# Kernel optimization log

Hardware: AMD Instinct MI355X
Metric: run time of the kernel (lower is better)

## Reference

```python
import jax, jax.numpy as jnp
import numpy as np

B, S, H, NH, HD, L, I, M = 2, 2048, 768, 12, 64, 6, 3072, 256
VOCAB, TYPES = 30522, 2
EPS = 1e-6  # layernorm epsilon and FAVOR+ numerical stabilizer


def layer_norm(x, g, b):
    mu = jnp.mean(x, axis=-1, keepdims=True)
    var = jnp.mean(jax.lax.square(x), axis=-1, keepdims=True) - jax.lax.square(mu)
    return (x - mu) * jax.lax.rsqrt(var + EPS) * g + b


def favor_attention(q, k, v, mask, proj):
    # q,k,v: [B,S,NH,HD]; proj: [M,HD] random features; mask: [B,S] float
    dn = 1.0 / np.sqrt(np.sqrt(HD))      # data normalizer for softmax kernel
    ratio = 1.0 / np.sqrt(M)
    qn, kn = q * dn, k * dn
    qp = jnp.einsum('bsnd,md->bsnm', qn, proj)
    kp = jnp.einsum('bsnd,md->bsnm', kn, proj)
    qd = 0.5 * jnp.sum(qn * qn, axis=-1, keepdims=True)
    kd = 0.5 * jnp.sum(kn * kn, axis=-1, keepdims=True)
    # stabilizers: per-position max for queries, global (seq+feature) max for keys
    q_prime = ratio * (jnp.exp(qp - qd - jnp.max(qp, axis=-1, keepdims=True)) + EPS)
    k_prime = ratio * (jnp.exp(kp - kd - jnp.max(kp, axis=(1, 3), keepdims=True)) + EPS)
    k_prime = k_prime * mask[:, :, None, None]
    kv = jnp.einsum('bsnm,bsnd->bnmd', k_prime, v)          # [B,NH,M,HD]
    num = jnp.einsum('bsnm,bnmd->bsnd', q_prime, kv)        # [B,S,NH,HD]
    den = jnp.einsum('bsnm,bnm->bsn', q_prime, jnp.sum(k_prime, axis=1))
    return num / den[..., None]


def setup_inputs() -> dict:
    key = jax.random.key(0)
    ks = jax.random.split(key, 32)
    f = lambda i, shape, s=0.02: (jax.random.normal(ks[i], shape, jnp.float32) * s)
    inp = {
        'input_ids': jax.random.randint(ks[0], (B, S), 0, VOCAB, jnp.int32),
        'token_type_ids': jax.random.randint(ks[1], (B, S), 0, TYPES, jnp.int32),
        'position_ids': jnp.tile(jnp.arange(S, dtype=jnp.int32)[None, :], (B, 1)),
        'attention_mask': jnp.ones((B, S), jnp.int32),
        'word_emb': f(2, (VOCAB, H), 0.1),
        'pos_emb': f(3, (S, H), 0.1),
        'type_emb': f(4, (TYPES, H), 0.1),
        'emb_ln_g': jnp.ones((H,), jnp.float32),
        'emb_ln_b': jnp.zeros((H,), jnp.float32),
        'wq': f(5, (L, H, NH, HD)), 'bq': jnp.zeros((L, NH, HD), jnp.float32),
        'wk': f(6, (L, H, NH, HD)), 'bk': jnp.zeros((L, NH, HD), jnp.float32),
        'wv': f(7, (L, H, NH, HD)), 'bv': jnp.zeros((L, NH, HD), jnp.float32),
        'wo': f(8, (L, NH, HD, H)), 'bo': jnp.zeros((L, H), jnp.float32),
        'ln1_g': jnp.ones((L, H), jnp.float32), 'ln1_b': jnp.zeros((L, H), jnp.float32),
        'wi': f(9, (L, H, I)), 'bi': jnp.zeros((L, I), jnp.float32),
        'wo2': f(10, (L, I, H)), 'bo2': jnp.zeros((L, H), jnp.float32),
        'ln2_g': jnp.ones((L, H), jnp.float32), 'ln2_b': jnp.zeros((L, H), jnp.float32),
        'proj': jax.random.normal(ks[11], (L, M, HD), jnp.float32),
    }
    return inp


def reference(input_ids, token_type_ids, position_ids, attention_mask,
              word_emb, pos_emb, type_emb, emb_ln_g, emb_ln_b,
              wq, bq, wk, bk, wv, bv, wo, bo, ln1_g, ln1_b,
              wi, bi, wo2, bo2, ln2_g, ln2_b, proj):
    mask = attention_mask.astype(jnp.float32)
    x = word_emb[input_ids] + pos_emb[position_ids] + type_emb[token_type_ids]
    x = layer_norm(x, emb_ln_g, emb_ln_b)
    for l in range(L):
        q = jnp.einsum('bsh,hnd->bsnd', x, wq[l]) + bq[l]
        k = jnp.einsum('bsh,hnd->bsnd', x, wk[l]) + bk[l]
        v = jnp.einsum('bsh,hnd->bsnd', x, wv[l]) + bv[l]
        att = favor_attention(q, k, v, mask, proj[l])
        att = jnp.einsum('bsnd,ndh->bsh', att, wo[l]) + bo[l]
        a = layer_norm(att + x, ln1_g[l], ln1_b[l])
        inter = jax.nn.gelu(jnp.einsum('bsh,hi->bsi', a, wi[l]) + bi[l])
        out = jnp.einsum('bsi,ih->bsh', inter, wo2[l]) + bo2[l]
        x = layer_norm(out + a, ln2_g[l], ln2_b[l])
    return x
```

## Files before the change

### kernel.cpp

```cpp
#include <hip/hip_runtime.h>
#include <hip/hip_bf16.h>

#define B_ 2
#define S_ 2048
#define H_ 768
#define NH_ 12
#define HD_ 64
#define L_ 6
#define I_ 3072
#define M_ 256
#define BS_ 4096
#define R_ 49152
#define NXH_ 3145728
#define EPS_ 1e-6f
#define DN_ 0.35355339059327373f
#define RATIO_ 0.0625f

typedef __attribute__((ext_vector_type(8))) short bf16x8;
typedef __attribute__((ext_vector_type(4))) float f32x4;

__device__ __forceinline__ void gload16(const void* g, void* l) {
    __builtin_amdgcn_global_load_lds(
        (const __attribute__((address_space(1))) void*)g,
        (__attribute__((address_space(3))) void*)l, 16, 0, 0);
}

__device__ __forceinline__ float gelu_f(float x) {
    const float c = 0.7978845608028654f;
    float x3 = x * x * x;
    return 0.5f * x * (1.0f + tanhf(c * (x + 0.044715f * x3)));
}

__device__ __forceinline__ void blockReduceSum2(float& a, float& b) {
    __shared__ float sa[4], sb[4];
    int lane = threadIdx.x & 63, wid = threadIdx.x >> 6;
    #pragma unroll
    for (int off = 32; off; off >>= 1) {
        a += __shfl_down(a, off, 64);
        b += __shfl_down(b, off, 64);
    }
    __syncthreads();
    if (lane == 0) { sa[wid] = a; sb[wid] = b; }
    __syncthreads();
    a = sa[0] + sa[1] + sa[2] + sa[3];
    b = sb[0] + sb[1] + sb[2] + sb[3];
    __syncthreads();
}

__device__ __forceinline__ float blockReduceMax(float v) {
    __shared__ float sm[4];
    int lane = threadIdx.x & 63, wid = threadIdx.x >> 6;
    #pragma unroll
    for (int off = 32; off; off >>= 1) v = fmaxf(v, __shfl_down(v, off, 64));
    __syncthreads();
    if (lane == 0) sm[wid] = v;
    __syncthreads();
    float r = fmaxf(fmaxf(sm[0], sm[1]), fmaxf(sm[2], sm[3]));
    __syncthreads();
    return r;
}

template<int ACT, int OUTMODE>
__global__ __launch_bounds__(256) void gemm_pipe3_kernel(
    const __hip_bfloat16* __restrict__ A, const __hip_bfloat16* __restrict__ BT,
    const float* __restrict__ bias, void* __restrict__ Cv,
    int K, int lda, int ldb, int ldc, float* __restrict__ aux)
{
    __shared__ __align__(16) unsigned short As[3][128][32];
    __shared__ __align__(16) unsigned short Bs[3][128][32];
    const int tid = threadIdx.x, lane = tid & 63, wid = tid >> 6;
    const int wr = wid >> 1, wc = wid & 1;
    const size_t r0 = (size_t)blockIdx.y * 128;
    const int n0 = blockIdx.x * 128;
    const size_t kbase = (size_t)blockIdx.z * (size_t)K;

    const int srow = lane >> 2;
    const int selem = ((lane & 3) ^ ((srow >> 1) & 3)) * 8;
    const unsigned short* ga0 = (const unsigned short*)A + (r0 + wid * 32 + srow) * (size_t)lda + kbase + selem;
    const unsigned short* gb0 = (const unsigned short*)BT + ((size_t)n0 + wid * 32 + srow) * (size_t)ldb + kbase + selem;

    f32x4 acc[4][4];
    #pragma unroll
    for (int i = 0; i < 4; i++)
        #pragma unroll
        for (int j = 0; j < 4; j++)
            acc[i][j] = (f32x4){0.f, 0.f, 0.f, 0.f};

    const int lr = lane & 15;
    const int rc8 = (((lane >> 4) ^ ((lr >> 1) & 3))) * 8;

#define STAGE_(t) { const int bb_ = (t) % 3; const int kk_ = (t) * 32;            \
    gload16(ga0 + kk_, &As[bb_][wid * 32][0]);                                    \
    gload16(ga0 + kk_ + 16 * (size_t)lda, &As[bb_][wid * 32 + 16][0]);            \
    gload16(gb0 + kk_, &Bs[bb_][wid * 32][0]);                                    \
    gload16(gb0 + kk_ + 16 * (size_t)ldb, &Bs[bb_][wid * 32 + 16][0]); }

#define ITER_(t, VMSTR, DOSTAGE) {                                                \
    if (DOSTAGE) STAGE_((t) + 2);                                                 \
    asm volatile("s_waitcnt vmcnt(" VMSTR ")" ::: "memory");                      \
    __builtin_amdgcn_sched_barrier(0);                                            \
    __builtin_amdgcn_s_barrier();                                                 \
    __builtin_amdgcn_sched_barrier(0);                                            \
    const int bb_ = (t) % 3;                                                      \
    bf16x8 af[4], bfv[4];                                                         \
    _Pragma("unroll") for (int i = 0; i < 4; i++)                                 \
        af[i] = *(const bf16x8*)&As[bb_][wr * 64 + i * 16 + lr][rc8];             \
    _Pragma("unroll") for (int j = 0; j < 4; j++)                                 \
        bfv[j] = *(const bf16x8*)&Bs[bb_][wc * 64 + j * 16 + lr][rc8];            \
    __builtin_amdgcn_s_setprio(1);                                                \
    _Pragma("unroll") for (int i = 0; i < 4; i++)                                 \
        _Pragma("unroll") for (int j = 0; j < 4; j++)                             \
            acc[i][j] = __builtin_amdgcn_mfma_f32_16x16x32_bf16(af[i], bfv[j], acc[i][j], 0, 0, 0); \
    __builtin_amdgcn_s_setprio(0);                                                \
    __builtin_amdgcn_s_barrier();                                                 \
    __builtin_amdgcn_sched_barrier(0); }

    const int nT = K >> 5;
    STAGE_(0); STAGE_(1);
    for (int t = 0; t < nT - 2; ++t) ITER_(t, "8", true);
    ITER_(nT - 2, "4", false);
    ITER_(nT - 1, "0", false);
#undef ITER_
#undef STAGE_

    const int rr = (lane >> 4) * 4;
    const int cc = lane & 15;
    if (OUTMODE == 3) {
        float* fpl = aux + (size_t)blockIdx.z * NXH_;
        #pragma unroll
        for (int i = 0; i < 4; i++) {
            #pragma unroll
            for (int j = 0; j < 4; j++) {
                size_t col = (size_t)n0 + wc * 64 + j * 16 + cc;
                #pragma unroll
                for (int rg = 0; rg < 4; rg++) {
                    size_t row = r0 + wr * 64 + i * 16 + rr + rg;
                    fpl[row * (size_t)ldc + col] = acc[i][j][rg];
                }
            }
        }
    } else if (OUTMODE == 1) {
        #pragma unroll
        for (int i = 0; i < 4; i++) {
            #pragma unroll
            for (int j = 0; j < 4; j++) {
                size_t col = (size_t)n0 + wc * 64 + j * 16 + cc;
                float bv_ = bias ? bias[col] : 0.f;
                #pragma unroll
                for (int rg = 0; rg < 4; rg++) {
                    size_t row = r0 + wr * 64 + i * 16 + rr + rg;
                    float v = acc[i][j][rg] + bv_;
                    if (ACT == 1) v = gelu_f(v);
                    ((__hip_bfloat16*)Cv)[row * (size_t)ldc + col] = __float2bfloat16(v);
                }
            }
        }
    } else {
        const size_t seg = (size_t)n0 / 768;
        const int colbase = n0 - (int)seg * 768;
        #pragma unroll
        for (int i = 0; i < 4; i++) {
            #pragma unroll
            for (int rg = 0; rg < 4; rg++) {
                size_t row = r0 + wr * 64 + i * 16 + rr + rg;
                float ss = 0.f;
                #pragma unroll
                for (int j = 0; j < 4; j++) {
                    int colw = wc * 64 + j * 16 + cc;
                    size_t col = (size_t)n0 + colw;
                    float bv_ = bias ? bias[col] : 0.f;
                    float v = acc[i][j][rg] + bv_;
                    __hip_bfloat16 hb = __float2bfloat16(v);
                    ((__hip_bfloat16*)Cv)[seg * (size_t)NXH_ + row * 768 + colbase + colw] = hb;
                    float vr = __bfloat162float(hb);
                    ss += vr * vr;
                }
                #pragma unroll
                for (int off = 1; off <= 8; off <<= 1)
                    ss += __shfl_xor(ss, off, 64);
                if (seg < 2 && (lane & 15) == 0) {
                    int nh = colbase / 64 + wc;
                    aux[seg * (size_t)R_ + row * 12 + nh] = 0.5f * DN_ * DN_ * ss;
                }
            }
        }
    }
}

__global__ __launch_bounds__(256) void gemm_pipe3_n64_kernel(
    const __hip_bfloat16* __restrict__ A, const __hip_bfloat16* __restrict__ BT,
    const float* __restrict__ bias, float* __restrict__ C,
    int K, int lda, int ldb, int ldc)
{
    __shared__ __align__(16) unsigned short As[3][128][32];
    __shared__ __align__(16) unsigned short Bs[3][64][32];
    const int tid = threadIdx.x, lane = tid & 63, wid = tid >> 6;
    const size_t r0 = (size_t)blockIdx.y * 128;
    const int n0 = blockIdx.x * 64;

    const int srow = lane >> 2;
    const int selem = ((lane & 3) ^ ((srow >> 1) & 3)) * 8;
    const unsigned short* ga0 = (const unsigned short*)A + (r0 + wid * 32 + srow) * (size_t)lda + selem;
    const unsigned short* gb0 = (const unsigned short*)BT + ((size_t)n0 + wid * 16 + srow) * (size_t)ldb + selem;

    f32x4 acc[2][4];
    #pragma unroll
    for (int i = 0; i < 2; i++)
        #pragma unroll
        for (int j = 0; j < 4; j++)
            acc[i][j] = (f32x4){0.f, 0.f, 0.f, 0.f};

    const int lr = lane & 15;
    const int rc8 = (((lane >> 4) ^ ((lr >> 1) & 3))) * 8;

#define STAGE_(t) { const int bb_ = (t) % 3; const int kk_ = (t) * 32;            \
    gload16(ga0 + kk_, &As[bb_][wid * 32][0]);                                    \
    gload16(ga0 + kk_ + 16 * (size_t)lda, &As[bb_][wid * 32 + 16][0]);            \
    gload16(gb0 + kk_, &Bs[bb_][wid * 16][0]); }

#define ITER_(t, VMSTR, DOSTAGE) {                                                \
    if (DOSTAGE) STAGE_((t) + 2);                                                 \
    asm volatile("s_waitcnt vmcnt(" VMSTR ")" ::: "memory");                      \
    __builtin_amdgcn_sched_barrier(0);                                            \
    __builtin_amdgcn_s_barrier();                                                 \
    __builtin_amdgcn_sched_barrier(0);                                            \
    const int bb_ = (t) % 3;                                                      \
    bf16x8 af[2], bfv[4];                                                         \
    _Pragma("unroll") for (int i = 0; i < 2; i++)                                 \
        af[i] = *(const bf16x8*)&As[bb_][wid * 32 + i * 16 + lr][rc8];            \
    _Pragma("unroll") for (int j = 0; j < 4; j++)                                 \
        bfv[j] = *(const bf16x8*)&Bs[bb_][j * 16 + lr][rc8];                      \
    __builtin_amdgcn_s_setprio(1);                                                \
    _Pragma("unroll") for (int i = 0; i < 2; i++)                                 \
        _Pragma("unroll") for (int j = 0; j < 4; j++)                             \
            acc[i][j] = __builtin_amdgcn_mfma_f32_16x16x32_bf16(af[i], bfv[j], acc[i][j], 0, 0, 0); \
    __builtin_amdgcn_s_setprio(0);                                                \
    __builtin_amdgcn_s_barrier();                                                 \
    __builtin_amdgcn_sched_barrier(0); }

    const int nT = K >> 5;
    STAGE_(0); STAGE_(1);
    for (int t = 0; t < nT - 2; ++t) ITER_(t, "6", true);
    ITER_(nT - 2, "3", false);
    ITER_(nT - 1, "0", false);
#undef ITER_
#undef STAGE_

    const int rr = (lane >> 4) * 4, cc = lane & 15;
    #pragma unroll
    for (int i = 0; i < 2; i++) {
        #pragma unroll
        for (int j = 0; j < 4; j++) {
            int col = n0 + j * 16 + cc;
            float bv_ = bias ? bias[col] : 0.f;
            #pragma unroll
            for (int rg = 0; rg < 4; rg++) {
                size_t row = r0 + wid * 32 + i * 16 + rr + rg;
                C[row * (size_t)ldc + col] = acc[i][j][rg] + bv_;
            }
        }
    }
}

__global__ __launch_bounds__(256) void gemm_projk_kernel(
    const __hip_bfloat16* __restrict__ A, const __hip_bfloat16* __restrict__ BT,
    __hip_bfloat16* __restrict__ Cv,
    int K, int lda, int ldb, int ldc, float alpha,
    float* __restrict__ rmaxp)
{
    __shared__ __align__(16) unsigned short As[2][128][32];
    __shared__ __align__(16) unsigned short Bs[2][128][32];
    __shared__ float rmx[128][2];
    const int tid = threadIdx.x, lane = tid & 63, wid = tid >> 6;
    const int wr = wid >> 1, wc = wid & 1;
    const size_t r0 = (size_t)blockIdx.y * 128;
    const int n0 = blockIdx.x * 128;

    const int srow = lane >> 2;
    const int selem = ((lane & 3) ^ ((srow >> 1) & 3)) * 8;
    const unsigned short* ga0 = (const unsigned short*)A + (r0 + wid * 32 + srow) * (size_t)lda + selem;
    const unsigned short* gb0 = (const unsigned short*)BT + ((size_t)n0 + wid * 32 + srow) * (size_t)ldb + selem;

    f32x4 acc[4][4];
    #pragma unroll
    for (int i = 0; i < 4; i++)
        #pragma unroll
        for (int j = 0; j < 4; j++)
            acc[i][j] = (f32x4){0.f, 0.f, 0.f, 0.f};

    gload16(ga0, &As[0][wid * 32][0]);
    gload16(ga0 + 16 * (size_t)lda, &As[0][wid * 32 + 16][0]);
    gload16(gb0, &Bs[0][wid * 32][0]);
    gload16(gb0 + 16 * (size_t)ldb, &Bs[0][wid * 32 + 16][0]);
    __syncthreads();

    const int lr = lane & 15;
    const int rc8 = (((lane >> 4) ^ ((lr >> 1) & 3))) * 8;

    int cur = 0;
    for (int k0 = 0; k0 < K; k0 += 32) {
        const int kn = k0 + 32;
        if (kn < K) {
            gload16(ga0 + kn, &As[cur ^ 1][wid * 32][0]);
            gload16(ga0 + kn + 16 * (size_t)lda, &As[cur ^ 1][wid * 32 + 16][0]);
            gload16(gb0 + kn, &Bs[cur ^ 1][wid * 32][0]);
            gload16(gb0 + kn + 16 * (size_t)ldb, &Bs[cur ^ 1][wid * 32 + 16][0]);
        }
        bf16x8 af[4], bfv[4];
        #pragma unroll
        for (int i = 0; i < 4; i++)
            af[i] = *(const bf16x8*)&As[cur][wr * 64 + i * 16 + lr][rc8];
        #pragma unroll
        for (int j = 0; j < 4; j++)
            bfv[j] = *(const bf16x8*)&Bs[cur][wc * 64 + j * 16 + lr][rc8];
        #pragma unroll
        for (int i = 0; i < 4; i++)
            #pragma unroll
            for (int j = 0; j < 4; j++)
                acc[i][j] = __builtin_amdgcn_mfma_f32_16x16x32_bf16(af[i], bfv[j], acc[i][j], 0, 0, 0);
        __syncthreads();
        cur ^= 1;
    }

    const int rr = (lane >> 4) * 4;
    const int cc = lane & 15;
    #pragma unroll
    for (int i = 0; i < 4; i++) {
        #pragma unroll
        for (int j = 0; j < 4; j++) {
            int colw = wc * 64 + j * 16 + cc;
            size_t col = (size_t)n0 + colw;
            #pragma unroll
            for (int rg = 0; rg < 4; rg++) {
                size_t row = r0 + wr * 64 + i * 16 + rr + rg;
                Cv[row * ldc + col] = __float2bfloat16(acc[i][j][rg] * alpha);
            }
        }
    }
    #pragma unroll
    for (int i = 0; i < 4; i++) {
        #pragma unroll
        for (int rg = 0; rg < 4; rg++) {
            float rm = -3.4e38f;
            #pragma unroll
            for (int j = 0; j < 4; j++) rm = fmaxf(rm, acc[i][j][rg] * alpha);
            #pragma unroll
            for (int off = 1; off <= 8; off <<= 1)
                rm = fmaxf(rm, __shfl_xor(rm, off, 64));
            if ((lane & 15) == 0) rmx[wr * 64 + i * 16 + rr + rg][wc] = rm;
        }
    }
    __syncthreads();
    if (tid < 128)
        rmaxp[(size_t)blockIdx.x * R_ + r0 + tid] = fmaxf(rmx[tid][0], rmx[tid][1]);
}

__global__ __launch_bounds__(512) void projq_den_kernel(
    const __hip_bfloat16* __restrict__ Qbp, const __hip_bfloat16* __restrict__ projb,
    const float* __restrict__ qd, const float* __restrict__ ksum,
    __hip_bfloat16* __restrict__ QPb, float* __restrict__ den)
{
    __shared__ __align__(16) unsigned short Asm[128][64];
    __shared__ __align__(16) unsigned short Bsm[256][64];
    __shared__ float ksl[12][256];
    __shared__ float red[128][4];
    __shared__ float rmaxv[128];
    __shared__ float qdl[128];
    const int tid = threadIdx.x, lane = tid & 63, w = tid >> 6;
    const int wrow = w >> 2, wcol = w & 3;
    const size_t r0 = (size_t)blockIdx.x * 128;
    const int b = (int)(r0 / 24576);

    #pragma unroll
    for (int it = 0; it < 6; it++) {
        int idx = tid + it * 512;
        ksl[idx >> 8][idx & 255] = ksum[((size_t)b * 12 + (idx >> 8)) * 256 + (idx & 255)];
    }
    if (tid < 128) qdl[tid] = qd[r0 + tid];

    const int lrow = lane >> 3, lch = lane & 7;
    const int sch = (lch ^ (lrow & 7)) * 8;
    #pragma unroll
    for (int it = 0; it < 2; it++) {
        int segr = (w * 2 + it) * 8;
        gload16((const unsigned short*)Qbp + (r0 + segr + lrow) * 64 + sch, &Asm[segr][0]);
    }
    #pragma unroll
    for (int it = 0; it < 4; it++) {
        int segr = (w * 4 + it) * 8;
        gload16((const unsigned short*)projb + (size_t)(segr + lrow) * 64 + sch, &Bsm[segr][0]);
    }
    __syncthreads();

    const int lr = lane & 15, kq = lane >> 4;
    f32x4 acc[4][4];
    #pragma unroll
    for (int i = 0; i < 4; i++)
        #pragma unroll
        for (int j = 0; j < 4; j++)
            acc[i][j] = (f32x4){0.f, 0.f, 0.f, 0.f};

    #pragma unroll
    for (int ks = 0; ks < 2; ks++) {
        const int ch = (((ks << 2) | kq) ^ (lr & 7)) * 8;
        bf16x8 af[4], bfv[4];
        #pragma unroll
        for (int i = 0; i < 4; i++)
            af[i] = *(const bf16x8*)&Asm[wrow * 64 + i * 16 + lr][ch];
        #pragma unroll
        for (int j = 0; j < 4; j++)
            bfv[j] = *(const bf16x8*)&Bsm[wcol * 64 + j * 16 + lr][ch];
        #pragma unroll
        for (int i = 0; i < 4; i++)
            #pragma unroll
            for (int j = 0; j < 4; j++)
                acc[i][j] = __builtin_amdgcn_mfma_f32_16x16x32_bf16(af[i], bfv[j], acc[i][j], 0, 0, 0);
    }

    #pragma unroll
    for (int i = 0; i < 4; i++) {
        #pragma unroll
        for (int rg = 0; rg < 4; rg++) {
            float rm = -3.4e38f;
            #pragma unroll
            for (int j = 0; j < 4; j++) rm = fmaxf(rm, acc[i][j][rg] * DN_);
            #pragma unroll
            for (int off = 1; off <= 8; off <<= 1)
                rm = fmaxf(rm, __shfl_xor(rm, off, 64));
            if ((lane & 15) == 0) red[wrow * 64 + i * 16 + kq * 4 + rg][wcol] = rm;
        }
    }
    __syncthreads();
    if (tid < 128)
        rmaxv[tid] = fmaxf(fmaxf(red[tid][0], red[tid][1]), fmaxf(red[tid][2], red[tid][3]));
    __syncthreads();

    #pragma unroll
    for (int i = 0; i < 4; i++) {
        #pragma unroll
        for (int rg = 0; rg < 4; rg++) {
            int row = wrow * 64 + i * 16 + kq * 4 + rg;
            size_t rglob = r0 + row;
            int nh = (int)(rglob % 12);
            float qdv = qdl[row], mx = rmaxv[row];
            float dsum = 0.f;
            #pragma unroll
            for (int j = 0; j < 4; j++) {
                int col = wcol * 64 + j * 16 + lr;
                float qp = acc[i][j][rg] * DN_;
                float qv = RATIO_ * (expf(qp - qdv - mx) + EPS_);
                __hip_bfloat16 qb = __float2bfloat16(qv);
                QPb[rglob * 256 + col] = qb;
                dsum += __bfloat162float(qb) * ksl[nh][col];
            }
            #pragma unroll
            for (int off = 1; off <= 8; off <<= 1)
                dsum += __shfl_xor(dsum, off, 64);
            if ((lane & 15) == 0) red[row][wcol] = dsum;
        }
    }
    __syncthreads();
    if (tid < 128)
        den[r0 + tid] = red[tid][0] + red[tid][1] + red[tid][2] + red[tid][3];
}

__global__ __launch_bounds__(256) void num_mfma_kernel(
    const __hip_bfloat16* __restrict__ QPb, const __hip_bfloat16* __restrict__ kvT,
    const float* __restrict__ den, __hip_bfloat16* __restrict__ ATT)
{
    __shared__ __align__(16) unsigned short As[2][128][32];
    __shared__ __align__(16) unsigned short Bs[2][64][32];
    const int tid = threadIdx.x, lane = tid & 63, wid = tid >> 6;
    const int s0 = blockIdx.x * 128;
    const int bn = blockIdx.y, b = bn / NH_, n = bn % NH_;

    const int srow = lane >> 2;
    const int selem = ((lane & 3) ^ ((srow >> 1) & 3)) * 8;
    const unsigned short* ga0 = (const unsigned short*)QPb + (size_t)b * S_ * (NH_ * M_) + n * M_
                              + ((size_t)s0 + wid * 32 + srow) * (NH_ * M_) + selem;
    const unsigned short* gb0 = (const unsigned short*)kvT + (size_t)bn * (HD_ * M_)
                              + ((size_t)wid * 16 + srow) * M_ + selem;

    f32x4 acc[2][4];
    #pragma unroll
    for (int i = 0; i < 2; i++)
        #pragma unroll
        for (int j = 0; j < 4; j++)
            acc[i][j] = (f32x4){0.f, 0.f, 0.f, 0.f};

    gload16(ga0, &As[0][wid * 32][0]);
    gload16(ga0 + 16 * (size_t)(NH_ * M_), &As[0][wid * 32 + 16][0]);
    gload16(gb0, &Bs[0][wid * 16][0]);
    __syncthreads();

    const int lr = lane & 15;
    const int rc8 = (((lane >> 4) ^ ((lr >> 1) & 3))) * 8;

    int cur = 0;
    for (int k0 = 0; k0 < M_; k0 += 32) {
        const int kn = k0 + 32;
        if (kn < M_) {
            gload16(ga0 + kn, &As[cur ^ 1][wid * 32][0]);
            gload16(ga0 + kn + 16 * (size_t)(NH_ * M_), &As[cur ^ 1][wid * 32 + 16][0]);
            gload16(gb0 + kn, &Bs[cur ^ 1][wid * 16][0]);
        }
        bf16x8 af[2], bfv[4];
        #pragma unroll
        for (int i = 0; i < 2; i++)
            af[i] = *(const bf16x8*)&As[cur][wid * 32 + i * 16 + lr][rc8];
        #pragma unroll
        for (int j = 0; j < 4; j++)
            bfv[j] = *(const bf16x8*)&Bs[cur][j * 16 + lr][rc8];
        #pragma unroll
        for (int i = 0; i < 2; i++)
            #pragma unroll
            for (int j = 0; j < 4; j++)
                acc[i][j] = __builtin_amdgcn_mfma_f32_16x16x32_bf16(af[i], bfv[j], acc[i][j], 0, 0, 0);
        __syncthreads();
        cur ^= 1;
    }

    const int rr = (lane >> 4) * 4, cc = lane & 15;
    #pragma unroll
    for (int i = 0; i < 2; i++) {
        #pragma unroll
        for (int rg = 0; rg < 4; rg++) {
            int s = s0 + wid * 32 + i * 16 + rr + rg;
            float inv = 1.0f / den[((size_t)b * S_ + s) * NH_ + n];
            #pragma unroll
            for (int j = 0; j < 4; j++)
                ATT[((size_t)b * S_ + s) * H_ + n * HD_ + j * 16 + cc]
                    = __float2bfloat16(acc[i][j][rg] * inv);
        }
    }
}

__global__ __launch_bounds__(256) void kv_fused_kernel(
    const __hip_bfloat16* __restrict__ KF, const __hip_bfloat16* __restrict__ Vb,
    const float* __restrict__ kd, const float* __restrict__ gmax,
    const int* __restrict__ amask,
    float* __restrict__ part, float* __restrict__ kpart)
{
    const int m0 = blockIdx.x * 64, bn = blockIdx.y, b = bn / NH_, n = bn % NH_;
    const int s0 = blockIdx.z * 256;
    __shared__ __align__(16) float As2[16][68];
    __shared__ __align__(16) float Bs2[16][68];
    __shared__ float sred[4][64];
    const int tid = threadIdx.x, tx = tid & 15, ty = tid >> 4;
    const float gm = gmax[bn];
    float acc[4][4] = {};
    float ks = 0.f;
    for (int ss = 0; ss < 256; ss += 16) {
        #pragma unroll
        for (int i = 0; i < 4; i++) {
            int idx = tid + i * 256;
            int kk = idx >> 6, c = idx & 63;
            size_t srow = (size_t)b * S_ + s0 + ss + kk;
            float kdv = kd[srow * 12 + n];
            float mk = (float)amask[srow];
            float kf = __bfloat162float(KF[srow * (NH_ * M_) + n * M_ + m0 + c]);
            float kp = RATIO_ * (expf(kf - kdv - gm) + EPS_) * mk;
            As2[kk][c] = kp;
            ks += kp;
            Bs2[kk][c] = __bfloat162float(Vb[srow * H_ + n * HD_ + c]);
        }
        __syncthreads();
        #pragma unroll
        for (int kk = 0; kk < 16; kk++) {
            float4 av = *reinterpret_cast<const float4*>(&As2[kk][ty * 4]);
            float4 bv = *reinterpret_cast<const float4*>(&Bs2[kk][tx * 4]);
            float a4[4] = {av.x, av.y, av.z, av.w};
            float b4[4] = {bv.x, bv.y, bv.z, bv.w};
            #pragma unroll
            for (int i = 0; i < 4; i++)
                #pragma unroll
                for (int j = 0; j < 4; j++)
                    acc[i][j] += a4[i] * b4[j];
        }
        __syncthreads();
    }
    float* Cb = part + ((size_t)blockIdx.z * (B_ * NH_) + bn) * (M_ * HD_);
    #pragma unroll
    for (int j = 0; j < 4; j++)
        #pragma unroll
        for (int i = 0; i < 4; i++)
            Cb[(size_t)(tx * 4 + j) * M_ + m0 + ty * 4 + i] = acc[i][j];
    sred[tid >> 6][tid & 63] = ks;
    __syncthreads();
    if (tid < 64)
        kpart[((size_t)bn * 8 + blockIdx.z) * M_ + m0 + tid]
            = sred[0][tid] + sred[1][tid] + sred[2][tid] + sred[3][tid];
}

__global__ __launch_bounds__(256) void kvred_kernel(
    const float* __restrict__ part, __hip_bfloat16* __restrict__ kvT)
{
    const int bn = blockIdx.x, d = blockIdx.y, m = threadIdx.x;
    float s = 0.f;
    #pragma unroll
    for (int c = 0; c < 8; c++)
        s += part[((size_t)c * (B_ * NH_) + bn) * (M_ * HD_) + (size_t)d * M_ + m];
    kvT[(size_t)bn * (HD_ * M_) + (size_t)d * M_ + m] = __float2bfloat16(s);
}

__global__ __launch_bounds__(256) void prep_kernel(
    const float* __restrict__ wq_l, const float* __restrict__ wk_l,
    const float* __restrict__ wv_l, const float* __restrict__ wo_l,
    const float* __restrict__ wi_l, const float* __restrict__ wo2_l,
    const float* __restrict__ proj_l,
    const float* __restrict__ bq_l, const float* __restrict__ bk_l, const float* __restrict__ bv_l,
    __hip_bfloat16* __restrict__ wqT, __hip_bfloat16* __restrict__ wkT,
    __hip_bfloat16* __restrict__ wvT, __hip_bfloat16* __restrict__ woT,
    __hip_bfloat16* __restrict__ wiT, __hip_bfloat16* __restrict__ wo2T,
    __hip_bfloat16* __restrict__ projb, float* __restrict__ biasq)
{
    __shared__ float tile[32][33];
    int bid = blockIdx.x;
    if (bid < 6912) {
        const float* src; __hip_bfloat16* dst; int K, N, kt, nt;
        if (bid < 2304) {
            int t = bid / 576, idx = bid % 576;
            src = (t == 0) ? wq_l : (t == 1) ? wk_l : (t == 2) ? wv_l : wo_l;
            dst = (t == 0) ? wqT : (t == 1) ? wkT : (t == 2) ? wvT : woT;
            K = 768; N = 768; kt = idx % 24; nt = idx / 24;
        } else if (bid < 4608) {
            int idx = bid - 2304;
            src = wi_l; dst = wiT; K = 768; N = 3072;
            kt = idx % 24; nt = idx / 24;
        } else {
            int idx = bid - 4608;
            src = wo2_l; dst = wo2T; K = 3072; N = 768;
            kt = idx % 96; nt = idx / 96;
        }
        int k0 = kt * 32, n0 = nt * 32;
        int tx = threadIdx.x & 31, ty = threadIdx.x >> 5;
        #pragma unroll
        for (int i = 0; i < 4; i++)
            tile[ty + i * 8][tx] = src[(size_t)(k0 + ty + i * 8) * N + n0 + tx];
        __syncthreads();
        #pragma unroll
        for (int i = 0; i < 4; i++)
            dst[(size_t)(n0 + ty + i * 8) * K + k0 + tx] = __float2bfloat16(tile[tx][ty + i * 8]);
    } else if (bid < 6976) {
        int i = (bid - 6912) * 256 + threadIdx.x;
        projb[i] = __float2bfloat16(proj_l[i]);
    } else {
        int i = (bid - 6976) * 256 + threadIdx.x;
        if (i < 768) biasq[i] = bq_l[i];
        else if (i < 1536) biasq[i] = bk_l[i - 768];
        else if (i < 2304) biasq[i] = bv_l[i - 1536];
    }
}

__global__ __launch_bounds__(256) void embed_ln_kernel(
    const int* __restrict__ ids, const int* __restrict__ tts, const int* __restrict__ pos,
    const float* __restrict__ wemb, const float* __restrict__ pemb, const float* __restrict__ temb,
    const float* __restrict__ g, const float* __restrict__ bb,
    float* __restrict__ out, __hip_bfloat16* __restrict__ outb)
{
    size_t row = blockIdx.x;
    int id = ids[row], tt = tts[row], ps = pos[row];
    const float* w0 = wemb + (size_t)id * H_;
    const float* p0 = pemb + (size_t)ps * H_;
    const float* t0 = temb + (size_t)tt * H_;
    float vals[3], s1 = 0.f, s2 = 0.f;
    #pragma unroll
    for (int i = 0; i < 3; i++) {
        int h = threadIdx.x + i * 256;
        float v = w0[h] + p0[h] + t0[h];
        vals[i] = v; s1 += v; s2 += v * v;
    }
    blockReduceSum2(s1, s2);
    float mu = s1 * (1.0f / H_);
    float var = s2 * (1.0f / H_) - mu * mu;
    float rs = rsqrtf(var + EPS_);
    #pragma unroll
    for (int i = 0; i < 3; i++) {
        int h = threadIdx.x + i * 256;
        float y = (vals[i] - mu) * rs * g[h] + bb[h];
        out[row * H_ + h] = y;
        outb[row * H_ + h] = __float2bfloat16(y);
    }
}

__global__ __launch_bounds__(256) void add_ln_kernel(
    const float* __restrict__ P, const float* __restrict__ Q,
    const float* __restrict__ g, const float* __restrict__ bb,
    float* __restrict__ out, __hip_bfloat16* __restrict__ outb)
{
    size_t row = blockIdx.x;
    float vals[3], s1 = 0.f, s2 = 0.f;
    #pragma unroll
    for (int i = 0; i < 3; i++) {
        int h = threadIdx.x + i * 256;
        float v = P[row * H_ + h] + Q[row * H_ + h];
        vals[i] = v; s1 += v; s2 += v * v;
    }
    blockReduceSum2(s1, s2);
    float mu = s1 * (1.0f / H_);
    float var = s2 * (1.0f / H_) - mu * mu;
    float rs = rsqrtf(var + EPS_);
    #pragma unroll
    for (int i = 0; i < 3; i++) {
        int h = threadIdx.x + i * 256;
        float y = (vals[i] - mu) * rs * g[h] + bb[h];
        out[row * H_ + h] = y;
        if (outb) outb[row * H_ + h] = __float2bfloat16(y);
    }
}

__global__ __launch_bounds__(256) void add_ln3_kernel(
    const float* __restrict__ planes, const float* __restrict__ bias,
    const float* __restrict__ Q,
    const float* __restrict__ g, const float* __restrict__ bb,
    float* __restrict__ out, __hip_bfloat16* __restrict__ outb)
{
    size_t row = blockIdx.x;
    float vals[3], s1 = 0.f, s2 = 0.f;
    #pragma unroll
    for (int i = 0; i < 3; i++) {
        int h = threadIdx.x + i * 256;
        size_t e = row * H_ + h;
        float v = planes[e] + planes[NXH_ + e] + bias[h] + Q[e];
        vals[i] = v; s1 += v; s2 += v * v;
    }
    blockReduceSum2(s1, s2);
    float mu = s1 * (1.0f / H_);
    float var = s2 * (1.0f / H_) - mu * mu;
    float rs = rsqrtf(var + EPS_);
    #pragma unroll
    for (int i = 0; i < 3; i++) {
        int h = threadIdx.x + i * 256;
        float y = (vals[i] - mu) * rs * g[h] + bb[h];
        out[row * H_ + h] = y;
        outb[row * H_ + h] = __float2bfloat16(y);
    }
}

__global__ __launch_bounds__(256) void gmax_kernel(
    const float* __restrict__ rmaxp, float* __restrict__ gmax)
{
    int bn = blockIdx.x, b = bn / NH_, n = bn % NH_;
    float mx = -3.4e38f;
    for (int s = threadIdx.x; s < S_; s += 256) {
        size_t r = ((size_t)b * S_ + s) * NH_ + n;
        mx = fmaxf(mx, fmaxf(rmaxp[r], rmaxp[R_ + r]));
    }
    mx = blockReduceMax(mx);
    if (threadIdx.x == 0) gmax[bn] = mx;
}

__global__ __launch_bounds__(256) void ksum_final_kernel(
    const float* __restrict__ part, float* __restrict__ ksum)
{
    int bn = blockIdx.x, m = threadIdx.x;
    float s = 0.f;
    #pragma unroll
    for (int c = 0; c < 8; c++) s += part[((size_t)bn * 8 + c) * M_ + m];
    ksum[(size_t)bn * M_ + m] = s;
}

extern "C" void kernel_launch(void* const* d_in, const int* in_sizes, int n_in,
                              void* d_out, int out_size, void* d_ws, size_t ws_size,
                              hipStream_t stream)
{
    const int* input_ids  = (const int*)d_in[0];
    const int* token_type = (const int*)d_in[1];
    const int* position   = (const int*)d_in[2];
    const int* amask      = (const int*)d_in[3];
    const float* wemb = (const float*)d_in[4];
    const float* pemb = (const float*)d_in[5];
    const float* temb = (const float*)d_in[6];
    const float* elng = (const float*)d_in[7];
    const float* elnb = (const float*)d_in[8];
    const float* wq  = (const float*)d_in[9];
    const float* bq  = (const float*)d_in[10];
    const float* wk  = (const float*)d_in[11];
    const float* bk  = (const float*)d_in[12];
    const float* wv  = (const float*)d_in[13];
    const float* bv  = (const float*)d_in[14];
    const float* wo  = (const float*)d_in[15];
    const float* bo  = (const float*)d_in[16];
    const float* ln1g = (const float*)d_in[17];
    const float* ln1b = (const float*)d_in[18];
    const float* wi  = (const float*)d_in[19];
    const float* bi  = (const float*)d_in[20];
    const float* wo2 = (const float*)d_in[21];
    const float* bo2 = (const float*)d_in[22];
    const float* ln2g = (const float*)d_in[23];
    const float* ln2b = (const float*)d_in[24];
    const float* proj = (const float*)d_in[25];

    float* ws = (float*)d_ws;
    float* X    = ws;
    float* T2   = X + 3145728;
    float* BIG  = T2 + 3145728;
    float* U    = BIG + 12582912;
    __hip_bfloat16* Xb  = (__hip_bfloat16*)(U + 6291456);
    __hip_bfloat16* Qb  = (__hip_bfloat16*)((float*)Xb + 1572864);
    __hip_bfloat16* Kb  = Qb + 3145728;
    __hip_bfloat16* Vb  = Kb + 3145728;
    __hip_bfloat16* BF1 = Vb + 3145728;
    __hip_bfloat16* WT  = BF1 + 3145728;
    float* kvT_f = (float*)(WT + 7094272);
    __hip_bfloat16* kvT = (__hip_bfloat16*)kvT_f;
    float* KSUM  = kvT_f + 196608;
    float* KPART = KSUM + 6144;
    float* RMAXP = KPART + 196608;
    float* GMAX  = RMAXP + 98304;
    float* QD    = GMAX + 64;
    float* KD    = QD + 49152;
    float* DEN   = KD + 49152;
    float* BIASQ = DEN + 49152;
    float* T1    = (float*)d_out;

    __hip_bfloat16* wqT  = WT;
    __hip_bfloat16* wkT  = wqT + 589824;
    __hip_bfloat16* wvT  = wkT + 589824;
    __hip_bfloat16* woT  = wvT + 589824;
    __hip_bfloat16* wiT  = woT + 589824;
    __hip_bfloat16* wo2T = wiT + 2359296;
    __hip_bfloat16* projb = wo2T + 2359296;
    __hip_bfloat16* QPb = (__hip_bfloat16*)U;
    float* PART = U;
    float* PLANES = U;
    __hip_bfloat16* BIGb = (__hip_bfloat16*)BIG;

    embed_ln_kernel<<<BS_, 256, 0, stream>>>(input_ids, token_type, position,
        wemb, pemb, temb, elng, elnb, X, Xb);

    for (int l = 0; l < L_; l++) {
        const float* wq_l = wq + (size_t)l * H_ * NH_ * HD_;
        const float* wk_l = wk + (size_t)l * H_ * NH_ * HD_;
        const float* wv_l = wv + (size_t)l * H_ * NH_ * HD_;
        const float* wo_l = wo + (size_t)l * NH_ * HD_ * H_;
        const float* bq_l = bq + (size_t)l * NH_ * HD_;
        const float* bk_l = bk + (size_t)l * NH_ * HD_;
        const float* bv_l = bv + (size_t)l * NH_ * HD_;
        const float* bo_l = bo + (size_t)l * H_;
        const float* wi_l = wi + (size_t)l * H_ * I_;
        const float* bi_l = bi + (size_t)l * I_;
        const float* wo2_l = wo2 + (size_t)l * I_ * H_;
        const float* bo2_l = bo2 + (size_t)l * H_;
        const float* proj_l = proj + (size_t)l * M_ * HD_;

        prep_kernel<<<6985, 256, 0, stream>>>(wq_l, wk_l, wv_l, wo_l, wi_l, wo2_l, proj_l,
            bq_l, bk_l, bv_l, wqT, wkT, wvT, woT, wiT, wo2T, projb, BIASQ);

        gemm_pipe3_kernel<0,2><<<dim3(18,32), 256, 0, stream>>>(
            Xb, wqT, BIASQ, (void*)Qb, 768, 768, 768, 768, QD);

        gemm_projk_kernel<<<dim3(2,384), 256, 0, stream>>>(
            Kb, projb, BIGb, 64, 64, 64, 256, DN_, RMAXP);
        gmax_kernel<<<B_*NH_, 256, 0, stream>>>(RMAXP, GMAX);
        kv_fused_kernel<<<dim3(4, B_*NH_, 8), 256, 0, stream>>>(
            BIGb, Vb, KD, GMAX, amask, PART, KPART);
        ksum_final_kernel<<<B_*NH_, 256, 0, stream>>>(KPART, KSUM);
        kvred_kernel<<<dim3(B_*NH_, HD_), 256, 0, stream>>>(PART, kvT);

        projq_den_kernel<<<384, 512, 0, stream>>>(Qb, projb, QD, KSUM, QPb, DEN);
        num_mfma_kernel<<<dim3(16, B_*NH_), 256, 0, stream>>>(QPb, kvT, DEN, BF1);

        gemm_pipe3_n64_kernel<<<dim3(12,32), 256, 0, stream>>>(
            BF1, woT, bo_l, T1, 768, 768, 768, 768);
        add_ln_kernel<<<BS_, 256, 0, stream>>>(T1, X, ln1g + (size_t)l*H_, ln1b + (size_t)l*H_, T2, BF1);

        gemm_pipe3_kernel<1,1><<<dim3(24,32), 256, 0, stream>>>(
            BF1, wiT, bi_l, (void*)BIGb, 768, 768, 768, 3072, nullptr);

        gemm_pipe3_kernel<0,3><<<dim3(6,32,2), 256, 0, stream>>>(
            BIGb, wo2T, nullptr, nullptr, 1536, 3072, 3072, 768, PLANES);
        float* xout = (l == L_ - 1) ? (float*)d_out : X;
        add_ln3_kernel<<<BS_, 256, 0, stream>>>(PLANES, bo2_l, T2,
            ln2g + (size_t)l*H_, ln2b + (size_t)l*H_, xout, Xb);
    }
}
```

Before: 1.685 ms.

## Fuse query feature map with numerator GEMM and replace gmax kernel with atomics

Merges the query random-feature projection/denominator kernel with the numerator MFMA kernel so the bf16 q' tile stays in LDS instead of being written to and re-read from global memory. It also folds the global key max into the projk GEMM epilogue using an order-preserving uint encoding with atomicMax, which removes the separate gmax kernel and its partial-max buffer. The atomic slot is reset in an extra prep block. The cost is a larger LDS footprint per block, which may reduce occupancy, and atomic contention on 24 addresses.

```diff
diff --git a/kernel.cpp b/kernel.cpp
--- a/kernel.cpp
+++ b/kernel.cpp
@@ -31,6 +31,14 @@
     return 0.5f * x * (1.0f + tanhf(c * (x + 0.044715f * x3)));
 }
 
+__device__ __forceinline__ unsigned enc_f(float f) {
+    unsigned u = __float_as_uint(f);
+    return (u & 0x80000000u) ? ~u : (u | 0x80000000u);
+}
+__device__ __forceinline__ float dec_f(unsigned u) {
+    return (u & 0x80000000u) ? __uint_as_float(u & 0x7fffffffu) : __uint_as_float(~u);
+}
+
 __device__ __forceinline__ void blockReduceSum2(float& a, float& b) {
     __shared__ float sa[4], sb[4];
     int lane = threadIdx.x & 63, wid = threadIdx.x >> 6;
@@ -45,19 +53,6 @@
     a = sa[0] + sa[1] + sa[2] + sa[3];
     b = sb[0] + sb[1] + sb[2] + sb[3];
     __syncthreads();
-}
-
-__device__ __forceinline__ float blockReduceMax(float v) {
-    __shared__ float sm[4];
-    int lane = threadIdx.x & 63, wid = threadIdx.x >> 6;
-    #pragma unroll
-    for (int off = 32; off; off >>= 1) v = fmaxf(v, __shfl_down(v, off, 64));
-    __syncthreads();
-    if (lane == 0) sm[wid] = v;
-    __syncthreads();
-    float r = fmaxf(fmaxf(sm[0], sm[1]), fmaxf(sm[2], sm[3]));
-    __syncthreads();
-    return r;
 }
 
 template<int ACT, int OUTMODE>
@@ -266,11 +261,12 @@
     const __hip_bfloat16* __restrict__ A, const __hip_bfloat16* __restrict__ BT,
     __hip_bfloat16* __restrict__ Cv,
     int K, int lda, int ldb, int ldc, float alpha,
-    float* __restrict__ rmaxp)
+    unsigned* __restrict__ gmaxu)
 {
     __shared__ __align__(16) unsigned short As[2][128][32];
     __shared__ __align__(16) unsigned short Bs[2][128][32];
     __shared__ float rmx[128][2];
+    __shared__ float rowm[128];
     const int tid = threadIdx.x, lane = tid & 63, wid = tid >> 6;
     const int wr = wid >> 1, wc = wid & 1;
     const size_t r0 = (size_t)blockIdx.y * 128;
@@ -351,44 +347,56 @@
         }
     }
     __syncthreads();
-    if (tid < 128)
-        rmaxp[(size_t)blockIdx.x * R_ + r0 + tid] = fmaxf(rmx[tid][0], rmx[tid][1]);
-}
-
-__global__ __launch_bounds__(512) void projq_den_kernel(
+    if (tid < 128) rowm[tid] = fmaxf(rmx[tid][0], rmx[tid][1]);
+    __syncthreads();
+    if (tid < 12) {
+        int b = (int)(r0 / 24576);
+        int h = (int)((r0 + tid) % 12);
+        float m = -3.4e38f;
+        for (int k = tid; k < 128; k += 12) m = fmaxf(m, rowm[k]);
+        atomicMax(&gmaxu[b * 12 + h], enc_f(m));
+    }
+}
+
+__global__ __launch_bounds__(512) void qnum_fused_kernel(
     const __hip_bfloat16* __restrict__ Qbp, const __hip_bfloat16* __restrict__ projb,
     const float* __restrict__ qd, const float* __restrict__ ksum,
-    __hip_bfloat16* __restrict__ QPb, float* __restrict__ den)
-{
-    __shared__ __align__(16) unsigned short Asm[128][64];
-    __shared__ __align__(16) unsigned short Bsm[256][64];
-    __shared__ float ksl[12][256];
+    const __hip_bfloat16* __restrict__ kvT, __hip_bfloat16* __restrict__ ATT)
+{
+    __shared__ __align__(16) unsigned short Pl[128][256];
+    __shared__ __align__(16) unsigned short kvTl[64][256];
+    __shared__ float ksl[256];
+    __shared__ float qdl[128];
     __shared__ float red[128][4];
     __shared__ float rmaxv[128];
-    __shared__ float qdl[128];
+    __shared__ float deni[128];
+    unsigned short (*Asm)[64] = (unsigned short (*)[64])&Pl[0][0];
+    unsigned short (*Bsm)[64] = (unsigned short (*)[64])(&Pl[0][0] + 8192);
+
     const int tid = threadIdx.x, lane = tid & 63, w = tid >> 6;
     const int wrow = w >> 2, wcol = w & 3;
-    const size_t r0 = (size_t)blockIdx.x * 128;
-    const int b = (int)(r0 / 24576);
-
-    #pragma unroll
-    for (int it = 0; it < 6; it++) {
-        int idx = tid + it * 512;
-        ksl[idx >> 8][idx & 255] = ksum[((size_t)b * 12 + (idx >> 8)) * 256 + (idx & 255)];
-    }
-    if (tid < 128) qdl[tid] = qd[r0 + tid];
+    const int bn = blockIdx.y, b = bn / NH_, n = bn % NH_;
+    const size_t r0g = (size_t)b * S_ + (size_t)blockIdx.x * 128;
+
+    if (tid < 256) ksl[tid] = ksum[(size_t)bn * 256 + tid];
+    else if (tid < 384) qdl[tid - 256] = qd[(r0g + tid - 256) * 12 + n];
 
     const int lrow = lane >> 3, lch = lane & 7;
     const int sch = (lch ^ (lrow & 7)) * 8;
-    #pragma unroll
-    for (int it = 0; it < 2; it++) {
-        int segr = (w * 2 + it) * 8;
-        gload16((const unsigned short*)Qbp + (r0 + segr + lrow) * 64 + sch, &Asm[segr][0]);
-    }
-    #pragma unroll
-    for (int it = 0; it < 4; it++) {
-        int segr = (w * 4 + it) * 8;
-        gload16((const unsigned short*)projb + (size_t)(segr + lrow) * 64 + sch, &Bsm[segr][0]);
+    gload16((const unsigned short*)Qbp + (r0g + w * 16 + lrow) * 768 + n * 64 + sch, &Asm[w * 16][0]);
+    gload16((const unsigned short*)Qbp + (r0g + w * 16 + 8 + lrow) * 768 + n * 64 + sch, &Asm[w * 16 + 8][0]);
+    #pragma unroll
+    for (int p = 0; p < 4; p++)
+        gload16((const unsigned short*)projb + (size_t)(w * 32 + p * 8 + lrow) * 64 + sch,
+                &Bsm[w * 32 + p * 8][0]);
+    {
+        const int rIn = lane >> 5, c32 = lane & 31;
+        #pragma unroll
+        for (int p = 0; p < 4; p++) {
+            int d = w * 8 + p * 2 + rIn;
+            gload16((const unsigned short*)kvT + (size_t)bn * (HD_ * M_) + (size_t)d * 256
+                    + (c32 ^ (d & 7)) * 8, &kvTl[w * 8 + p * 2][0]);
+        }
     }
     __syncthreads();
 
@@ -440,8 +448,6 @@
         #pragma unroll
         for (int rg = 0; rg < 4; rg++) {
             int row = wrow * 64 + i * 16 + kq * 4 + rg;
-            size_t rglob = r0 + row;
-            int nh = (int)(rglob % 12);
             float qdv = qdl[row], mx = rmaxv[row];
             float dsum = 0.f;
             #pragma unroll
@@ -450,8 +456,8 @@
                 float qp = acc[i][j][rg] * DN_;
                 float qv = RATIO_ * (expf(qp - qdv - mx) + EPS_);
                 __hip_bfloat16 qb = __float2bfloat16(qv);
-                QPb[rglob * 256 + col] = qb;
-                dsum += __bfloat162float(qb) * ksl[nh][col];
+                Pl[row][((col >> 3) ^ (row & 7)) * 8 + (col & 7)] = *(unsigned short*)&qb;
+                dsum += __bfloat162float(qb) * ksl[col];
             }
             #pragma unroll
             for (int off = 1; off <= 8; off <<= 1)
@@ -461,83 +467,37 @@
     }
     __syncthreads();
     if (tid < 128)
-        den[r0 + tid] = red[tid][0] + red[tid][1] + red[tid][2] + red[tid][3];
-}
-
-__global__ __launch_bounds__(256) void num_mfma_kernel(
-    const __hip_bfloat16* __restrict__ QPb, const __hip_bfloat16* __restrict__ kvT,
-    const float* __restrict__ den, __hip_bfloat16* __restrict__ ATT)
-{
-    __shared__ __align__(16) unsigned short As[2][128][32];
-    __shared__ __align__(16) unsigned short Bs[2][64][32];
-    const int tid = threadIdx.x, lane = tid & 63, wid = tid >> 6;
-    const int s0 = blockIdx.x * 128;
-    const int bn = blockIdx.y, b = bn / NH_, n = bn % NH_;
-
-    const int srow = lane >> 2;
-    const int selem = ((lane & 3) ^ ((srow >> 1) & 3)) * 8;
-    const unsigned short* ga0 = (const unsigned short*)QPb + (size_t)b * S_ * (NH_ * M_) + n * M_
-                              + ((size_t)s0 + wid * 32 + srow) * (NH_ * M_) + selem;
-    const unsigned short* gb0 = (const unsigned short*)kvT + (size_t)bn * (HD_ * M_)
-                              + ((size_t)wid * 16 + srow) * M_ + selem;
-
-    f32x4 acc[2][4];
-    #pragma unroll
-    for (int i = 0; i < 2; i++)
+        deni[tid] = red[tid][0] + red[tid][1] + red[tid][2] + red[tid][3];
+    __syncthreads();
+
+    f32x4 acc2[4];
+    #pragma unroll
+    for (int j = 0; j < 4; j++) acc2[j] = (f32x4){0.f, 0.f, 0.f, 0.f};
+    #pragma unroll
+    for (int ks = 0; ks < 8; ks++) {
+        const int mc = ks * 4 + kq;
+        const int sl = (mc ^ (lr & 7)) * 8;
+        bf16x8 af = *(const bf16x8*)&Pl[w * 16 + lr][sl];
+        #pragma unroll
+        for (int j = 0; j < 4; j++) {
+            bf16x8 bfv = *(const bf16x8*)&kvTl[j * 16 + lr][sl];
+            acc2[j] = __builtin_amdgcn_mfma_f32_16x16x32_bf16(af, bfv, acc2[j], 0, 0, 0);
+        }
+    }
+    #pragma unroll
+    for (int rg = 0; rg < 4; rg++) {
+        int row = w * 16 + kq * 4 + rg;
+        float inv = 1.0f / deni[row];
         #pragma unroll
         for (int j = 0; j < 4; j++)
-            acc[i][j] = (f32x4){0.f, 0.f, 0.f, 0.f};
-
-    gload16(ga0, &As[0][wid * 32][0]);
-    gload16(ga0 + 16 * (size_t)(NH_ * M_), &As[0][wid * 32 + 16][0]);
-    gload16(gb0, &Bs[0][wid * 16][0]);
-    __syncthreads();
-
-    const int lr = lane & 15;
-    const int rc8 = (((lane >> 4) ^ ((lr >> 1) & 3))) * 8;
-
-    int cur = 0;
-    for (int k0 = 0; k0 < M_; k0 += 32) {
-        const int kn = k0 + 32;
-        if (kn < M_) {
-            gload16(ga0 + kn, &As[cur ^ 1][wid * 32][0]);
-            gload16(ga0 + kn + 16 * (size_t)(NH_ * M_), &As[cur ^ 1][wid * 32 + 16][0]);
-            gload16(gb0 + kn, &Bs[cur ^ 1][wid * 16][0]);
-        }
-        bf16x8 af[2], bfv[4];
-        #pragma unroll
-        for (int i = 0; i < 2; i++)
-            af[i] = *(const bf16x8*)&As[cur][wid * 32 + i * 16 + lr][rc8];
-        #pragma unroll
-        for (int j = 0; j < 4; j++)
-            bfv[j] = *(const bf16x8*)&Bs[cur][j * 16 + lr][rc8];
-        #pragma unroll
-        for (int i = 0; i < 2; i++)
-            #pragma unroll
-            for (int j = 0; j < 4; j++)
-                acc[i][j] = __builtin_amdgcn_mfma_f32_16x16x32_bf16(af[i], bfv[j], acc[i][j], 0, 0, 0);
-        __syncthreads();
-        cur ^= 1;
-    }
-
-    const int rr = (lane >> 4) * 4, cc = lane & 15;
-    #pragma unroll
-    for (int i = 0; i < 2; i++) {
-        #pragma unroll
-        for (int rg = 0; rg < 4; rg++) {
-            int s = s0 + wid * 32 + i * 16 + rr + rg;
-            float inv = 1.0f / den[((size_t)b * S_ + s) * NH_ + n];
-            #pragma unroll
-            for (int j = 0; j < 4; j++)
-                ATT[((size_t)b * S_ + s) * H_ + n * HD_ + j * 16 + cc]
-                    = __float2bfloat16(acc[i][j][rg] * inv);
-        }
+            ATT[(r0g + row) * 768 + n * 64 + j * 16 + lr]
+                = __float2bfloat16(acc2[j][rg] * inv);
     }
 }
 
 __global__ __launch_bounds__(256) void kv_fused_kernel(
     const __hip_bfloat16* __restrict__ KF, const __hip_bfloat16* __restrict__ Vb,
-    const float* __restrict__ kd, const float* __restrict__ gmax,
+    const float* __restrict__ kd, const unsigned* __restrict__ gmaxu,
     const int* __restrict__ amask,
     float* __restrict__ part, float* __restrict__ kpart)
 {
@@ -547,7 +507,7 @@
     __shared__ __align__(16) float Bs2[16][68];
     __shared__ float sred[4][64];
     const int tid = threadIdx.x, tx = tid & 15, ty = tid >> 4;
-    const float gm = gmax[bn];
+    const float gm = dec_f(gmaxu[bn]);
     float acc[4][4] = {};
     float ks = 0.f;
     for (int ss = 0; ss < 256; ss += 16) {
@@ -612,7 +572,8 @@
     __hip_bfloat16* __restrict__ wqT, __hip_bfloat16* __restrict__ wkT,
     __hip_bfloat16* __restrict__ wvT, __hip_bfloat16* __restrict__ woT,
     __hip_bfloat16* __restrict__ wiT, __hip_bfloat16* __restrict__ wo2T,
-    __hip_bfloat16* __restrict__ projb, float* __restrict__ biasq)
+    __hip_bfloat16* __restrict__ projb, float* __restrict__ biasq,
+    unsigned* __restrict__ gmaxu)
 {
     __shared__ float tile[32][33];
     int bid = blockIdx.x;
@@ -644,11 +605,13 @@
     } else if (bid < 6976) {
         int i = (bid - 6912) * 256 + threadIdx.x;
         projb[i] = __float2bfloat16(proj_l[i]);
-    } else {
+    } else if (bid < 6985) {
         int i = (bid - 6976) * 256 + threadIdx.x;
         if (i < 768) biasq[i] = bq_l[i];
         else if (i < 1536) biasq[i] = bk_l[i - 768];
         else if (i < 2304) biasq[i] = bv_l[i - 1536];
+    } else {
+        if (threadIdx.x < 24) gmaxu[threadIdx.x] = 0u;
     }
 }
 
@@ -735,19 +698,6 @@
         out[row * H_ + h] = y;
         outb[row * H_ + h] = __float2bfloat16(y);
     }
-}
-
-__global__ __launch_bounds__(256) void gmax_kernel(
-    const float* __restrict__ rmaxp, float* __restrict__ gmax)
-{
-    int bn = blockIdx.x, b = bn / NH_, n = bn % NH_;
-    float mx = -3.4e38f;
-    for (int s = threadIdx.x; s < S_; s += 256) {
-        size_t r = ((size_t)b * S_ + s) * NH_ + n;
-        mx = fmaxf(mx, fmaxf(rmaxp[r], rmaxp[R_ + r]));
-    }
-    mx = blockReduceMax(mx);
-    if (threadIdx.x == 0) gmax[bn] = mx;
 }
 
 __global__ __launch_bounds__(256) void ksum_final_kernel(
@@ -806,12 +756,11 @@
     __hip_bfloat16* kvT = (__hip_bfloat16*)kvT_f;
     float* KSUM  = kvT_f + 196608;
     float* KPART = KSUM + 6144;
-    float* RMAXP = KPART + 196608;
-    float* GMAX  = RMAXP + 98304;
-    float* QD    = GMAX + 64;
+    float* RSVD  = KPART + 196608;
+    unsigned* GMAXU = (unsigned*)(RSVD + 98304);
+    float* QD    = (float*)GMAXU + 64;
     float* KD    = QD + 49152;
-    float* DEN   = KD + 49152;
-    float* BIASQ = DEN + 49152;
+    float* BIASQ = KD + 49152;
     float* T1    = (float*)d_out;
 
     __hip_bfloat16* wqT  = WT;
@@ -821,7 +770,6 @@
     __hip_bfloat16* wiT  = woT + 589824;
     __hip_bfloat16* wo2T = wiT + 2359296;
     __hip_bfloat16* projb = wo2T + 2359296;
-    __hip_bfloat16* QPb = (__hip_bfloat16*)U;
     float* PART = U;
     float* PLANES = U;
     __hip_bfloat16* BIGb = (__hip_bfloat16*)BIG;
@@ -844,22 +792,21 @@
         const float* bo2_l = bo2 + (size_t)l * H_;
         const float* proj_l = proj + (size_t)l * M_ * HD_;
 
-        prep_kernel<<<6985, 256, 0, stream>>>(wq_l, wk_l, wv_l, wo_l, wi_l, wo2_l, proj_l,
-            bq_l, bk_l, bv_l, wqT, wkT, wvT, woT, wiT, wo2T, projb, BIASQ);
+        prep_kernel<<<6986, 256, 0, stream>>>(wq_l, wk_l, wv_l, wo_l, wi_l, wo2_l, proj_l,
+            bq_l, bk_l, bv_l, wqT, wkT, wvT, woT, wiT, wo2T, projb, BIASQ, GMAXU);
 
         gemm_pipe3_kernel<0,2><<<dim3(18,32), 256, 0, stream>>>(
             Xb, wqT, BIASQ, (void*)Qb, 768, 768, 768, 768, QD);
 
         gemm_projk_kernel<<<dim3(2,384), 256, 0, stream>>>(
-            Kb, projb, BIGb, 64, 64, 64, 256, DN_, RMAXP);
-        gmax_kernel<<<B_*NH_, 256, 0, stream>>>(RMAXP, GMAX);
+            Kb, projb, BIGb, 64, 64, 64, 256, DN_, GMAXU);
         kv_fused_kernel<<<dim3(4, B_*NH_, 8), 256, 0, stream>>>(
-            BIGb, Vb, KD, GMAX, amask, PART, KPART);
+            BIGb, Vb, KD, GMAXU, amask, PART, KPART);
         ksum_final_kernel<<<B_*NH_, 256, 0, stream>>>(KPART, KSUM);
         kvred_kernel<<<dim3(B_*NH_, HD_), 256, 0, stream>>>(PART, kvT);
 
-        projq_den_kernel<<<384, 512, 0, stream>>>(Qb, projb, QD, KSUM, QPb, DEN);
-        num_mfma_kernel<<<dim3(16, B_*NH_), 256, 0, stream>>>(QPb, kvT, DEN, BF1);
+        qnum_fused_kernel<<<dim3(16, B_*NH_), 512, 0, stream>>>(
+            Qb, projb, QD, KSUM, kvT, BF1);
 
         gemm_pipe3_n64_kernel<<<dim3(12,32), 256, 0, stream>>>(
             BF1, woT, bo_l, T1, 768, 768, 768, 768);
```

After: 1.631 ms. 1.03x faster.
